# Kernel optimization log

Measured on AMD Instinct MI355X. Metric: run time of the kernel, lower is better.

## Reference

```python
import jax, jax.numpy as jnp
import numpy as np

B, S, D = 8, 1024, 512          # batch, seq_len, embed_dim
H = 8                            # num_heads
KD = D                           # key_dim = embed_dim (per source)
DM = H * KD                      # internal d_model = 4096
FF = 2048                        # dense_dim
EPS = 1e-3                       # keras LayerNormalization default epsilon


def glorot(key, shape):
    fan_in, fan_out = shape[0], shape[1]
    lim = np.sqrt(6.0 / (fan_in + fan_out)).astype(np.float32)
    return jax.random.uniform(key, shape, jnp.float32, -lim, lim)


def setup_inputs() -> dict:
    key = jax.random.key(0)
    ks = jax.random.split(key, 8)
    return {
        "inputs": jax.random.normal(ks[0], (B, S, D), jnp.float32),
        "w_q": glorot(ks[1], (D, DM)), "b_q": jnp.zeros((DM,), jnp.float32),
        "w_k": glorot(ks[2], (D, DM)), "b_k": jnp.zeros((DM,), jnp.float32),
        "w_v": glorot(ks[3], (D, DM)), "b_v": jnp.zeros((DM,), jnp.float32),
        "w_o": glorot(ks[4], (DM, D)), "b_o": jnp.zeros((D,), jnp.float32),
        "w1": glorot(ks[5], (D, FF)), "b1": jnp.zeros((FF,), jnp.float32),
        "w2": glorot(ks[6], (FF, D)), "b2": jnp.zeros((D,), jnp.float32),
        "g1": jnp.ones((D,), jnp.float32), "beta1": jnp.zeros((D,), jnp.float32),
        "g2": jnp.ones((D,), jnp.float32), "beta2": jnp.zeros((D,), jnp.float32),
    }


def _layernorm(x, gamma, beta):
    mu = jnp.mean(x, axis=-1, keepdims=True)
    var = jnp.mean(jnp.square(x - mu), axis=-1, keepdims=True)
    return (x - mu) * jax.lax.rsqrt(var + EPS) * gamma + beta


def reference(inputs, w_q, b_q, w_k, b_k, w_v, b_v, w_o, b_o,
              w1, b1, w2, b2, g1, beta1, g2, beta2):
    # --- custom multi-head self-attention ---
    q = (inputs @ w_q + b_q).reshape(B, S, H, KD)   # [B,S,H,KD]
    k = (inputs @ w_k + b_k).reshape(B, S, H, KD)
    v = (inputs @ w_v + b_v).reshape(B, S, H, KD)
    scale = jnp.sqrt(jnp.float32(KD))
    scores = jnp.einsum("bqhd,bkhd->bhqk", q, k) / scale   # [B,H,S,S]
    attn = jax.nn.softmax(scores, axis=-1)
    ctx = jnp.einsum("bhqk,bkhd->bqhd", attn, v).reshape(B, S, DM)
    attn_out = ctx @ w_o + b_o                               # [B,S,D]
    # --- residual + LN 1 ---
    proj_in = _layernorm(inputs + attn_out, g1, beta1)
    # --- FFN ---
    ffn = jax.nn.relu(proj_in @ w1 + b1) @ w2 + b2
    # --- residual + LN 2 ---
    return _layernorm(proj_in + ffn, g2, beta2)
```

## Files before the change

### kernel.cpp

```cpp
#include <hip/hip_runtime.h>
#include <stdint.h>

typedef __bf16 bf16_t;
typedef bf16_t bf16x8 __attribute__((ext_vector_type(8)));
typedef float floatx4 __attribute__((ext_vector_type(4)));

__device__ __forceinline__ unsigned short f2bf(float f) {
  union { float f; uint32_t u; } v; v.f = f;
  return (unsigned short)((v.u + 0x7fffu + ((v.u >> 16) & 1u)) >> 16);
}

#define GLD16(g, l)                                                            \
  __builtin_amdgcn_global_load_lds(                                            \
      (const __attribute__((address_space(1))) void*)(g),                      \
      (__attribute__((address_space(3))) void*)(l), 16, 0, 0)

template <int BIAS_MODE, bool RELU, bool OUT_BF16>
__global__ __launch_bounds__(512, 2) void gemm256(
    const unsigned short* __restrict__ A, const unsigned short* __restrict__ Bt,
    void* __restrict__ C, const float* __restrict__ bias, int K, int lda,
    int ldb, int ldc, long sA, long sB, long sC) {
  __shared__ __align__(16) unsigned short As[2][256 * 64];
  __shared__ __align__(16) unsigned short Bs[2][256 * 64];
  const int tid = threadIdx.x;
  const int lane = tid & 63;
  const int wave = tid >> 6;
  const int quad = lane >> 4;
  const int l15 = lane & 15;
  const unsigned short* Ab = A + blockIdx.z * sA + (long)blockIdx.y * 256 * lda;
  const unsigned short* Bb = Bt + blockIdx.z * sB + (long)blockIdx.x * 256 * ldb;
  const int wm = (wave & 1) << 7;
  const int wn = (wave >> 1) << 6;

  floatx4 acc[8][4] = {};

  const int sr = tid >> 3;
  const int sc = tid & 7;
  const int NT = K >> 6;

  auto stage = [&](int t, int buf) {
    const int kt = t << 6;
#pragma unroll
    for (int i = 0; i < 4; ++i) {
      int r = sr + i * 64;
      int gc = sc ^ (r & 7);
      GLD16(Ab + (long)r * lda + kt + gc * 8,
            &As[buf][(i * 64 + (wave << 3)) * 64]);
    }
#pragma unroll
    for (int i = 0; i < 4; ++i) {
      int r = sr + i * 64;
      int gc = sc ^ (r & 7);
      GLD16(Bb + (long)r * ldb + kt + gc * 8,
            &Bs[buf][(i * 64 + (wave << 3)) * 64]);
    }
  };

  stage(0, 0);
  stage(1, 1);
  asm volatile("s_waitcnt vmcnt(8)\n\ts_barrier" ::: "memory");

  int cur = 0;
  for (int t = 0; t < NT; ++t) {
    const unsigned short* Ap = As[cur];
    const unsigned short* Bp = Bs[cur];
#pragma unroll
    for (int ih = 0; ih < 2; ++ih) {
      bf16x8 aF[4][2];
#pragma unroll
      for (int i4 = 0; i4 < 4; ++i4)
#pragma unroll
        for (int ks = 0; ks < 2; ++ks) {
          int row = wm + ih * 64 + i4 * 16 + l15;
          int sw = (ks * 4 + quad) ^ (row & 7);
          aF[i4][ks] = *(const bf16x8*)(Ap + row * 64 + sw * 8);
        }
#pragma unroll
      for (int jh = 0; jh < 2; ++jh) {
        bf16x8 bF[2][2];
#pragma unroll
        for (int j2 = 0; j2 < 2; ++j2)
#pragma unroll
          for (int ks = 0; ks < 2; ++ks) {
            int row = wn + jh * 32 + j2 * 16 + l15;
            int sw = (ks * 4 + quad) ^ (row & 7);
            bF[j2][ks] = *(const bf16x8*)(Bp + row * 64 + sw * 8);
          }
        __builtin_amdgcn_s_setprio(1);
#pragma unroll
        for (int j2 = 0; j2 < 2; ++j2)
#pragma unroll
          for (int i4 = 0; i4 < 4; ++i4)
#pragma unroll
            for (int ks = 0; ks < 2; ++ks)
              acc[ih * 4 + i4][jh * 2 + j2] =
                  __builtin_amdgcn_mfma_f32_16x16x32_bf16(
                      aF[i4][ks], bF[j2][ks], acc[ih * 4 + i4][jh * 2 + j2],
                      0, 0, 0);
        __builtin_amdgcn_s_setprio(0);
      }
    }
    if (t == NT - 1) break;
    asm volatile("s_waitcnt lgkmcnt(0)\n\ts_barrier" ::: "memory");
    if (t + 2 < NT) {
      stage(t + 2, cur);
      asm volatile("s_waitcnt vmcnt(8)\n\ts_barrier" ::: "memory");
    } else {
      asm volatile("s_waitcnt vmcnt(0)\n\ts_barrier" ::: "memory");
    }
    cur ^= 1;
  }

  const int rl = quad << 2;
  const int cl = l15;
#pragma unroll
  for (int i = 0; i < 8; ++i) {
#pragma unroll
    for (int j = 0; j < 4; ++j) {
#pragma unroll
      for (int rg = 0; rg < 4; ++rg) {
        int row = (blockIdx.y << 8) + wm + i * 16 + rl + rg;
        int col = (blockIdx.x << 8) + wn + j * 16 + cl;
        float v = acc[i][j][rg];
        if (BIAS_MODE == 1) v += bias[col];
        if (BIAS_MODE == 2) v += bias[row];
        if (RELU) v = fmaxf(v, 0.0f);
        long idx = blockIdx.z * sC + (long)row * ldc + col;
        if (OUT_BF16)
          ((unsigned short*)C)[idx] = f2bf(v);
        else
          ((float*)C)[idx] = v;
      }
    }
  }
}

__global__ __launch_bounds__(512, 2) void attn(
    const unsigned short* __restrict__ qk, const unsigned short* __restrict__ vt,
    unsigned short* __restrict__ ctx) {
  __shared__ unsigned short ldsK[2][32 * 512];
  __shared__ unsigned short ldsV[2][32 * 512];
  __shared__ unsigned short ldsP[128 * 40];
  __shared__ float ldsL[128];

  const int tid = threadIdx.x;
  const int lane = tid & 63;
  const int wave = tid >> 6;
  const int quad = lane >> 4;
  const int l15 = lane & 15;
  const int b = blockIdx.x >> 3;
  const int h = blockIdx.x & 7;
  const int qblk = blockIdx.y << 7;
  const float cs = 0.044194173824159216f * 1.4426950408889634f;

  bf16x8 qf[16];
  {
    const unsigned short* qp =
        qk + (long)(b * 1024 + qblk + wave * 16 + l15) * 8192 + h * 512 +
        (quad << 3);
#pragma unroll
    for (int ks = 0; ks < 16; ++ks) qf[ks] = *(const bf16x8*)(qp + ks * 32);
  }

  floatx4 o[32];
#pragma unroll
  for (int i = 0; i < 32; ++i) o[i] = floatx4{0.f, 0.f, 0.f, 0.f};
  floatx4 l_i = floatx4{0.f, 0.f, 0.f, 0.f};

  const int st_d = lane >> 2;
  const int st_kc = ((lane & 3) - (lane >> 3)) & 3;

  {
#pragma unroll
    for (int i = 0; i < 4; ++i) {
      int r = i * 8 + wave;
      int gc = (lane & ~7) | ((lane ^ r) & 7);
      GLD16(qk + (long)(b * 1024 + r) * 8192 + 4096 + h * 512 + gc * 8,
            ldsK[0] + r * 512);
    }
#pragma unroll
    for (int i = 0; i < 4; ++i) {
      int j = i * 8 + wave;
      GLD16(vt + (long)(b * 4096 + h * 512 + j * 16 + st_d) * 1024 + st_kc * 8,
            ldsV[0] + j * 512);
    }
  }
  __syncthreads();

  for (int kt = 0; kt < 32; ++kt) {
    const unsigned short* kb = ldsK[kt & 1];
    const unsigned short* vb = ldsV[kt & 1];
    if (kt + 1 < 32) {
#pragma unroll
      for (int i = 0; i < 4; ++i) {
        int r = i * 8 + wave;
        int gc = (lane & ~7) | ((lane ^ r) & 7);
        GLD16(qk + (long)(b * 1024 + (kt + 1) * 32 + r) * 8192 + 4096 +
                  h * 512 + gc * 8,
              ldsK[(kt + 1) & 1] + r * 512);
      }
#pragma unroll
      for (int i = 0; i < 4; ++i) {
        int j = i * 8 + wave;
        GLD16(vt + (long)(b * 4096 + h * 512 + j * 16 + st_d) * 1024 +
                  (kt + 1) * 32 + st_kc * 8,
              ldsV[(kt + 1) & 1] + j * 512);
      }
    }

    floatx4 s0 = floatx4{0.f, 0.f, 0.f, 0.f}, s1 = floatx4{0.f, 0.f, 0.f, 0.f};
#pragma unroll
    for (int ks = 0; ks < 16; ++ks) {
      int ch = ks * 4 + quad;
      int sw = (ch & ~7) | ((ch ^ l15) & 7);
      bf16x8 k0 = *(const bf16x8*)(kb + l15 * 512 + sw * 8);
      bf16x8 k1 = *(const bf16x8*)(kb + (16 + l15) * 512 + sw * 8);
      s0 = __builtin_amdgcn_mfma_f32_16x16x32_bf16(qf[ks], k0, s0, 0, 0, 0);
      s1 = __builtin_amdgcn_mfma_f32_16x16x32_bf16(qf[ks], k1, s1, 0, 0, 0);
    }

    {
      unsigned short* pw = ldsP + wave * 16 * 40;
      const int rb = quad << 2;
#pragma unroll
      for (int r = 0; r < 4; ++r) {
        float e0 = __builtin_amdgcn_exp2f(s0[r] * cs);
        float e1 = __builtin_amdgcn_exp2f(s1[r] * cs);
        l_i[r] += e0 + e1;
        pw[(rb + r) * 40 + l15] = f2bf(e0);
        pw[(rb + r) * 40 + 16 + l15] = f2bf(e1);
      }
    }
    asm volatile("s_waitcnt lgkmcnt(0)\n\ts_barrier" ::: "memory");

#pragma unroll
    for (int half = 0; half < 2; ++half) {
      bf16x8 pf[4];
#pragma unroll
      for (int q4 = 0; q4 < 4; ++q4)
        pf[q4] = *(const bf16x8*)(ldsP + ((half * 4 + q4) * 16 + l15) * 40 +
                                  (quad << 3));
#pragma unroll
      for (int db = 0; db < 4; ++db) {
        int n = wave * 4 + db;
        bf16x8 vf = *(const bf16x8*)(
            vb + n * 512 + (l15 * 4 + ((quad + (l15 >> 1)) & 3)) * 8);
#pragma unroll
        for (int q4 = 0; q4 < 4; ++q4)
          o[(half * 4 + q4) * 4 + db] = __builtin_amdgcn_mfma_f32_16x16x32_bf16(
              pf[q4], vf, o[(half * 4 + q4) * 4 + db], 0, 0, 0);
      }
    }
    __syncthreads();
  }

#pragma unroll
  for (int r = 0; r < 4; ++r) {
    float rs = l_i[r];
    rs += __shfl_xor(rs, 1);
    rs += __shfl_xor(rs, 2);
    rs += __shfl_xor(rs, 4);
    rs += __shfl_xor(rs, 8);
    if (l15 == 0) ldsL[wave * 16 + (quad << 2) + r] = rs;
  }
  __syncthreads();

#pragma unroll
  for (int qb = 0; qb < 8; ++qb) {
    floatx4 lv = *(const floatx4*)(ldsL + qb * 16 + (quad << 2));
    floatx4 inv;
#pragma unroll
    for (int r = 0; r < 4; ++r) inv[r] = 1.0f / lv[r];
#pragma unroll
    for (int db = 0; db < 4; ++db) {
#pragma unroll
      for (int r = 0; r < 4; ++r) {
        long row = (long)(b * 1024 + qblk + qb * 16 + (quad << 2) + r);
        ctx[row * 4096 + h * 512 + wave * 64 + db * 16 + l15] =
            f2bf(o[qb * 4 + db][r] * inv[r]);
      }
    }
  }
}

template <bool WB>
__global__ __launch_bounds__(256) void ln_reduce(
    const float* __restrict__ p, long sP, const float* __restrict__ bias,
    const float* __restrict__ resid, const float* __restrict__ gamma,
    const float* __restrict__ beta, float* __restrict__ of,
    unsigned short* __restrict__ ob) {
  const long row = blockIdx.x;
  const int c = threadIdx.x * 2;
  const float2 a0 = ((const float2*)(p + row * 512))[threadIdx.x];
  const float2 a1 = ((const float2*)(p + sP + row * 512))[threadIdx.x];
  const float2 a2 = ((const float2*)(p + 2 * sP + row * 512))[threadIdx.x];
  const float2 a3 = ((const float2*)(p + 3 * sP + row * 512))[threadIdx.x];
  const float2 rv = ((const float2*)(resid + row * 512))[threadIdx.x];
  const float x0 = a0.x + a1.x + a2.x + a3.x + bias[c] + rv.x;
  const float x1 = a0.y + a1.y + a2.y + a3.y + bias[c + 1] + rv.y;
  float s = x0 + x1;
  float ss = x0 * x0 + x1 * x1;
#pragma unroll
  for (int d = 1; d < 64; d <<= 1) {
    s += __shfl_xor(s, d);
    ss += __shfl_xor(ss, d);
  }
  __shared__ float ps[4], pq[4];
  const int wave = threadIdx.x >> 6;
  if ((threadIdx.x & 63) == 0) {
    ps[wave] = s;
    pq[wave] = ss;
  }
  __syncthreads();
  s = ps[0] + ps[1] + ps[2] + ps[3];
  ss = pq[0] + pq[1] + pq[2] + pq[3];
  const float mu = s * (1.0f / 512.0f);
  const float rstd = rsqrtf(ss * (1.0f / 512.0f) - mu * mu + 1e-3f);
  const float y0 = (x0 - mu) * rstd * gamma[c] + beta[c];
  const float y1 = (x1 - mu) * rstd * gamma[c + 1] + beta[c + 1];
  ((float2*)(of + row * 512))[threadIdx.x] = make_float2(y0, y1);
  if (WB) {
    ushort2 o2;
    o2.x = f2bf(y0);
    o2.y = f2bf(y1);
    ((ushort2*)(ob + row * 512))[threadIdx.x] = o2;
  }
}

__global__ __launch_bounds__(256) void cast_bf16(const float* __restrict__ in,
                                                 unsigned short* __restrict__ out,
                                                 int n) {
  int i = (blockIdx.x * 256 + threadIdx.x) * 4;
  if (i < n) {
    float4 v = *(const float4*)(in + i);
    ushort4 o;
    o.x = f2bf(v.x);
    o.y = f2bf(v.y);
    o.z = f2bf(v.z);
    o.w = f2bf(v.w);
    *(ushort4*)(out + i) = o;
  }
}

__global__ __launch_bounds__(256) void transpose_cast(const float* __restrict__ in,
                                                      unsigned short* __restrict__ out,
                                                      int R, int C) {
  __shared__ float tile[32][33];
  const int tx = threadIdx.x & 31, ty = threadIdx.x >> 5;
  const int c0 = blockIdx.x * 32, r0 = blockIdx.y * 32;
#pragma unroll
  for (int i = 0; i < 4; ++i)
    tile[ty + i * 8][tx] = in[(long)(r0 + ty + i * 8) * C + c0 + tx];
  __syncthreads();
#pragma unroll
  for (int i = 0; i < 4; ++i)
    out[(long)(c0 + ty + i * 8) * R + r0 + tx] = f2bf(tile[tx][ty + i * 8]);
}

extern "C" void kernel_launch(void* const* d_in, const int* in_sizes, int n_in,
                              void* d_out, int out_size, void* d_ws,
                              size_t ws_size, hipStream_t stream) {
  const float* x = (const float*)d_in[0];
  const float* w_q = (const float*)d_in[1];
  const float* b_q = (const float*)d_in[2];
  const float* w_k = (const float*)d_in[3];
  const float* b_k = (const float*)d_in[4];
  const float* w_v = (const float*)d_in[5];
  const float* b_v = (const float*)d_in[6];
  const float* w_o = (const float*)d_in[7];
  const float* b_o = (const float*)d_in[8];
  const float* w1 = (const float*)d_in[9];
  const float* b1 = (const float*)d_in[10];
  const float* w2 = (const float*)d_in[11];
  const float* b2 = (const float*)d_in[12];
  const float* g1 = (const float*)d_in[13];
  const float* be1 = (const float*)d_in[14];
  const float* g2 = (const float*)d_in[15];
  const float* be2 = (const float*)d_in[16];
  float* out = (float*)d_out;

  char* ws = (char*)d_ws;
  size_t off = 0;
  auto alloc = [&](size_t n) {
    char* p = ws + off;
    off += (n + 255) & ~(size_t)255;
    return p;
  };
  unsigned short* xb = (unsigned short*)alloc(8192ll * 512 * 2);
  unsigned short* wqk_t = (unsigned short*)alloc(8192ll * 512 * 2);
  unsigned short* wv_t = (unsigned short*)alloc(4096ll * 512 * 2);
  unsigned short* wo_t = (unsigned short*)alloc(512ll * 4096 * 2);
  unsigned short* w1_t = (unsigned short*)alloc(2048ll * 512 * 2);
  unsigned short* w2_t = (unsigned short*)alloc(512ll * 2048 * 2);
  float* bqk = (float*)alloc(8192ll * 4);
  unsigned short* qkb = (unsigned short*)alloc(4096ll * 8192 * 2);
  unsigned short* vtb = (unsigned short*)alloc(4ll * 4096 * 1024 * 2);
  unsigned short* ctxf = (unsigned short*)alloc(8192ll * 4096 * 2);
  float* proj = (float*)alloc(8192ll * 512 * 4);
  unsigned short* projb = xb;
  unsigned short* h1 = qkb;
  float* pOP = (float*)qkb;
  float* pF2 = (float*)ctxf;

  hipMemcpyAsync(bqk, b_q, 4096 * 4, hipMemcpyDeviceToDevice, stream);
  hipMemcpyAsync(bqk + 4096, b_k, 4096 * 4, hipMemcpyDeviceToDevice, stream);

  cast_bf16<<<4096, 256, 0, stream>>>(x, xb, 8192 * 512);
  transpose_cast<<<dim3(128, 16), 256, 0, stream>>>(w_q, wqk_t, 512, 4096);
  transpose_cast<<<dim3(128, 16), 256, 0, stream>>>(w_k, wqk_t + 4096ll * 512, 512, 4096);
  transpose_cast<<<dim3(128, 16), 256, 0, stream>>>(w_v, wv_t, 512, 4096);
  transpose_cast<<<dim3(16, 128), 256, 0, stream>>>(w_o, wo_t, 4096, 512);
  transpose_cast<<<dim3(64, 16), 256, 0, stream>>>(w1, w1_t, 512, 2048);
  transpose_cast<<<dim3(16, 64), 256, 0, stream>>>(w2, w2_t, 2048, 512);

  for (int g = 0; g < 2; ++g) {
    const unsigned short* xg = xb + (long)g * 4096 * 512;
    gemm256<1, false, true><<<dim3(32, 16, 1), 512, 0, stream>>>(
        xg, wqk_t, qkb, bqk, 512, 512, 512, 8192, 0, 0, 0);
    gemm256<2, false, true><<<dim3(4, 16, 4), 512, 0, stream>>>(
        wv_t, xg, vtb, b_v, 512, 512, 512, 1024, 0, 1024ll * 512,
        4096ll * 1024);
    attn<<<dim3(32, 8), 512, 0, stream>>>(qkb, vtb, ctxf + (long)g * 4096 * 4096);
  }
  gemm256<0, false, false><<<dim3(2, 32, 4), 512, 0, stream>>>(
      ctxf, wo_t, pOP, nullptr, 1024, 4096, 4096, 512, 1024, 1024,
      8192ll * 512);
  ln_reduce<true><<<8192, 256, 0, stream>>>(pOP, 8192ll * 512, b_o, x, g1, be1,
                                            proj, projb);
  gemm256<1, true, true><<<dim3(8, 32, 1), 512, 0, stream>>>(
      projb, w1_t, h1, b1, 512, 512, 512, 2048, 0, 0, 0);
  gemm256<0, false, false><<<dim3(2, 32, 4), 512, 0, stream>>>(
      h1, w2_t, pF2, nullptr, 512, 2048, 2048, 512, 512, 512, 8192ll * 512);
  ln_reduce<false><<<8192, 256, 0, stream>>>(pF2, 8192ll * 512, b2, proj, g2,
                                             be2, out, nullptr);
}
```

Before: 507.2 us.

## Software-pipeline attention loop: overlap QK^T of tile t with PV of tile t-1

Restructures the attention kernel's key-tile loop into a skewed software pipeline. Each iteration prefetches K for t+1 and V for t, computes QK^T and exp for tile t into a double-buffered P tile, then does PV for tile t-1, so there is one barrier per iteration instead of two. This targets the stall between score computation and the PV MFMAs and the extra barrier. In exchange it adds a second P buffer in LDS and a prologue and epilogue, and it delays the V loads by one stage.

```diff
diff --git a/kernel.cpp b/kernel.cpp
--- a/kernel.cpp
+++ b/kernel.cpp
@@ -140,7 +140,7 @@
     unsigned short* __restrict__ ctx) {
   __shared__ unsigned short ldsK[2][32 * 512];
   __shared__ unsigned short ldsV[2][32 * 512];
-  __shared__ unsigned short ldsP[128 * 40];
+  __shared__ unsigned short ldsP[2][128 * 40];
   __shared__ float ldsL[128];
 
   const int tid = threadIdx.x;
@@ -170,44 +170,27 @@
   const int st_d = lane >> 2;
   const int st_kc = ((lane & 3) - (lane >> 3)) & 3;
 
-  {
+  auto stageK = [&](int t) {
 #pragma unroll
     for (int i = 0; i < 4; ++i) {
       int r = i * 8 + wave;
       int gc = (lane & ~7) | ((lane ^ r) & 7);
-      GLD16(qk + (long)(b * 1024 + r) * 8192 + 4096 + h * 512 + gc * 8,
-            ldsK[0] + r * 512);
-    }
+      GLD16(qk + (long)(b * 1024 + t * 32 + r) * 8192 + 4096 + h * 512 +
+                gc * 8,
+            ldsK[t & 1] + r * 512);
+    }
+  };
+  auto stageV = [&](int t) {
 #pragma unroll
     for (int i = 0; i < 4; ++i) {
       int j = i * 8 + wave;
-      GLD16(vt + (long)(b * 4096 + h * 512 + j * 16 + st_d) * 1024 + st_kc * 8,
-            ldsV[0] + j * 512);
-    }
-  }
-  __syncthreads();
-
-  for (int kt = 0; kt < 32; ++kt) {
-    const unsigned short* kb = ldsK[kt & 1];
-    const unsigned short* vb = ldsV[kt & 1];
-    if (kt + 1 < 32) {
-#pragma unroll
-      for (int i = 0; i < 4; ++i) {
-        int r = i * 8 + wave;
-        int gc = (lane & ~7) | ((lane ^ r) & 7);
-        GLD16(qk + (long)(b * 1024 + (kt + 1) * 32 + r) * 8192 + 4096 +
-                  h * 512 + gc * 8,
-              ldsK[(kt + 1) & 1] + r * 512);
-      }
-#pragma unroll
-      for (int i = 0; i < 4; ++i) {
-        int j = i * 8 + wave;
-        GLD16(vt + (long)(b * 4096 + h * 512 + j * 16 + st_d) * 1024 +
-                  (kt + 1) * 32 + st_kc * 8,
-              ldsV[(kt + 1) & 1] + j * 512);
-      }
-    }
-
+      GLD16(vt + (long)(b * 4096 + h * 512 + j * 16 + st_d) * 1024 + t * 32 +
+                st_kc * 8,
+            ldsV[t & 1] + j * 512);
+    }
+  };
+  auto qkt_sm = [&](int t) {
+    const unsigned short* kb = ldsK[t & 1];
     floatx4 s0 = floatx4{0.f, 0.f, 0.f, 0.f}, s1 = floatx4{0.f, 0.f, 0.f, 0.f};
 #pragma unroll
     for (int ks = 0; ks < 16; ++ks) {
@@ -218,27 +201,26 @@
       s0 = __builtin_amdgcn_mfma_f32_16x16x32_bf16(qf[ks], k0, s0, 0, 0, 0);
       s1 = __builtin_amdgcn_mfma_f32_16x16x32_bf16(qf[ks], k1, s1, 0, 0, 0);
     }
-
-    {
-      unsigned short* pw = ldsP + wave * 16 * 40;
-      const int rb = quad << 2;
-#pragma unroll
-      for (int r = 0; r < 4; ++r) {
-        float e0 = __builtin_amdgcn_exp2f(s0[r] * cs);
-        float e1 = __builtin_amdgcn_exp2f(s1[r] * cs);
-        l_i[r] += e0 + e1;
-        pw[(rb + r) * 40 + l15] = f2bf(e0);
-        pw[(rb + r) * 40 + 16 + l15] = f2bf(e1);
-      }
-    }
-    asm volatile("s_waitcnt lgkmcnt(0)\n\ts_barrier" ::: "memory");
-
+    unsigned short* pw = ldsP[t & 1] + wave * 16 * 40;
+    const int rb = quad << 2;
+#pragma unroll
+    for (int r = 0; r < 4; ++r) {
+      float e0 = __builtin_amdgcn_exp2f(s0[r] * cs);
+      float e1 = __builtin_amdgcn_exp2f(s1[r] * cs);
+      l_i[r] += e0 + e1;
+      pw[(rb + r) * 40 + l15] = f2bf(e0);
+      pw[(rb + r) * 40 + 16 + l15] = f2bf(e1);
+    }
+  };
+  auto pv = [&](int t) {
+    const unsigned short* pb = ldsP[t & 1];
+    const unsigned short* vb = ldsV[t & 1];
 #pragma unroll
     for (int half = 0; half < 2; ++half) {
       bf16x8 pf[4];
 #pragma unroll
       for (int q4 = 0; q4 < 4; ++q4)
-        pf[q4] = *(const bf16x8*)(ldsP + ((half * 4 + q4) * 16 + l15) * 40 +
+        pf[q4] = *(const bf16x8*)(pb + ((half * 4 + q4) * 16 + l15) * 40 +
                                   (quad << 3));
 #pragma unroll
       for (int db = 0; db < 4; ++db) {
@@ -251,8 +233,19 @@
               pf[q4], vf, o[(half * 4 + q4) * 4 + db], 0, 0, 0);
       }
     }
-    __syncthreads();
-  }
+  };
+
+  stageK(0);
+  asm volatile("s_waitcnt vmcnt(0)\n\ts_barrier" ::: "memory");
+
+  for (int t = 0; t < 32; ++t) {
+    if (t + 1 < 32) stageK(t + 1);
+    stageV(t);
+    qkt_sm(t);
+    if (t > 0) pv(t - 1);
+    asm volatile("s_waitcnt vmcnt(0) lgkmcnt(0)\n\ts_barrier" ::: "memory");
+  }
+  pv(31);
 
 #pragma unroll
   for (int r = 0; r < 4; ++r) {
```

Measured after the change: 568.7 us. +12.1%, slower.
